# Performance work log

Measured on AMD Instinct MI355X. Metric: run time of the kernel, lower is better.

## Reference

```python
import jax, jax.numpy as jnp
import numpy as np

TAU = 0.07          # softmax temperature
THR = 0.3           # Jaccard similarity threshold for positive pairs
EPS_NORM = 1e-12    # F.normalize eps


def setup_inputs() -> dict:
    key = jax.random.key(0)
    k1, k2, k3 = jax.random.split(key, 3)
    N, D, A = 4096, 128, 512
    z1 = jax.random.normal(k1, (N, D), dtype=jnp.float32)
    z2 = jax.random.normal(k2, (N, D), dtype=jnp.float32)
    labels = jax.random.randint(k3, (N, A), 0, 2).astype(jnp.int32)
    return {"z1": z1, "z2": z2, "labels": labels}


def _l2_normalize(x):
    n = jnp.linalg.norm(x, axis=-1, keepdims=True)
    return x / jnp.maximum(n, EPS_NORM)


def reference(z1, z2, labels):
    # Implements the N > 1000 (chunked) branch of SupConLoss.forward,
    # vectorized over all anchors at once (chunking is just tiling; math identical).
    N = z1.shape[0]
    idx = jnp.arange(N)

    z1n = _l2_normalize(z1)                       # (N, D)
    z2n = _l2_normalize(z2)                       # (N, D)
    z_all = jnp.concatenate([z1n, z2n], axis=0)   # (2N, D)

    # Jaccard label similarity -> positive-pair mask
    lab = labels.astype(jnp.float32)              # (N, A)
    inter = lab @ lab.T                           # (N, N)
    s = lab.sum(axis=1, keepdims=True)            # (N, 1)
    union = s + s.T - inter
    jaccard = inter / (union + 1e-8)
    pos_label = jaccard >= THR                    # (N, N) bool

    # pos mask over 2N columns: label-positives in both halves,
    # augmented view [j, N+j] forced True, self column [j, j] forced False.
    pos_mask = jnp.concatenate([pos_label, pos_label], axis=1)  # (N, 2N)
    pos_mask = pos_mask.at[idx, N + idx].set(True)
    pos_mask = pos_mask.at[idx, idx].set(False)

    # similarity of z1 anchors against all 2N embeddings
    sim = (z1n @ z_all.T) / TAU                   # (N, 2N)
    sim = sim - jax.lax.stop_gradient(sim.max(axis=1, keepdims=True))
    exp_sim = jnp.exp(sim)

    # denominator excludes the self column [j, j]
    denom = exp_sim.sum(axis=1, keepdims=True) - exp_sim[idx, idx][:, None]
    log_prob = sim - jnp.log(denom + 1e-8)

    num_pos = jnp.maximum(pos_mask.sum(axis=1), 1)
    loss_per_sample = -jnp.where(pos_mask, log_prob, 0.0).sum(axis=1) / num_pos
    return loss_per_sample.sum() / N
```

## Files before the change

### kernel.cpp

```cpp
#include <hip/hip_runtime.h>
#include <math.h>

#define N_ROWS 4096
#define DIM    128
#define A_LAB  512
#define INV_TAU 14.285714285714286f
#define C_EXP   20.609929155556620f

typedef __attribute__((ext_vector_type(8))) short short8;
typedef __attribute__((ext_vector_type(4))) float f32x4;
typedef __attribute__((ext_vector_type(4))) int i32x4;
typedef __attribute__((ext_vector_type(16))) int i32x16;


__device__ __forceinline__ unsigned short f2bf(float f) {
  unsigned int u = __builtin_bit_cast(unsigned int, f);
  u += 0x7fffu + ((u >> 16) & 1u);
  return (unsigned short)(u >> 16);
}

__global__ __launch_bounds__(256) void k_norm_pack(
    const float* __restrict__ z1, const float* __restrict__ z2,
    const int* __restrict__ labels,
    unsigned int* __restrict__ zbf, uint2* __restrict__ labs8,
    int* __restrict__ s, float* __restrict__ part, float* __restrict__ out)
{
  {
    const int idx = blockIdx.x * 256 + threadIdx.x;
    if (idx < 3 * 4096) part[idx] = 0.0f;
    if (idx == 0) out[0] = 0.0f;
  }
  const int wave = threadIdx.x >> 6, lane = threadIdx.x & 63;
  const int r = blockIdx.x * 4 + wave;
  const float* src = (r < N_ROWS) ? (z1 + (size_t)r * DIM)
                                  : (z2 + (size_t)(r - N_ROWS) * DIM);
  float2 x = ((const float2*)src)[lane];
  float ss = x.x * x.x + x.y * x.y;
  #pragma unroll
  for (int off = 32; off > 0; off >>= 1) ss += __shfl_xor(ss, off);
  const float inv = 1.0f / fmaxf(sqrtf(ss), 1e-12f);
  const unsigned int lo = f2bf(x.x * inv);
  const unsigned int hi = f2bf(x.y * inv);
  {
    const int u = lane >> 2, p = lane & 3;
    const int kf = u >> 2, quad = u & 3;
    const int g = r >> 4;
    zbf[(size_t)(((g * 4 + kf) * 64) + ((r & 15) + (quad << 4))) * 4 + p] = (hi << 16) | lo;
  }

  if (r < N_ROWS) {
    const int4* lp = (const int4*)(labels + (size_t)r * A_LAB);
    const int4 a = lp[2 * lane], b = lp[2 * lane + 1];
    const unsigned int w0 = (unsigned int)(a.x != 0)       | ((unsigned int)(a.y != 0) << 8)
                          | ((unsigned int)(a.z != 0) << 16) | ((unsigned int)(a.w != 0) << 24);
    const unsigned int w1 = (unsigned int)(b.x != 0)       | ((unsigned int)(b.y != 0) << 8)
                          | ((unsigned int)(b.z != 0) << 16) | ((unsigned int)(b.w != 0) << 24);
    uint2 v; v.x = w0; v.y = w1;
    const int ul = lane >> 1, hp = lane & 1;
    const int ks = ul >> 1, h = ul & 1;
    const int g = r >> 5;
    labs8[(size_t)(((g * 16 + ks) * 64) + ((r & 31) + (h << 5))) * 2 + hp] = v;
    int cnt = __popc(w0) + __popc(w1);
    #pragma unroll
    for (int off = 32; off > 0; off >>= 1) cnt += __shfl_xor(cnt, off);
    if (lane == 0) s[r] = cnt;
  }
}

__global__ __launch_bounds__(512, 4) void k_jac(
    const unsigned char* __restrict__ labs8, const int* __restrict__ s,
    unsigned int* __restrict__ pm)
{
  int r = blockIdx.x, row = 0;
  while (r >= 32 - row) { r -= 32 - row; ++row; }
  const int bi = row, bj = row + r;
  const int ibase = bi * 128, jbase = bj * 128;
  const bool diag = (bi == bj);

  const int tid = threadIdx.x;
  const int wave = tid >> 6, lane = tid & 63;
  const char* gl = (const char*)labs8;

  const int jwr = (wave >> 2) * 64;
  const int jwc = (wave & 3) * 32;
  const int col32 = lane & 31, h = lane >> 5;

  const int s3i = 3 * s[ibase + jwr + lane];
  const int s3j = 3 * s[jbase + jwc + col32];

  i32x16 jacc[2];
  #pragma unroll
  for (int rt = 0; rt < 2; ++rt)
    #pragma unroll
    for (int e = 0; e < 16; ++e) jacc[rt][e] = 0;

  const int gI = (ibase + jwr) >> 5;
  const int gJ = (jbase + jwc) >> 5;
  #pragma unroll
  for (int ks = 0; ks < 16; ++ks) {
    i32x4 a[2], b;
    #pragma unroll
    for (int rt = 0; rt < 2; ++rt)
      a[rt] = *(const i32x4*)(gl + (size_t)(((gI + rt) * 16 + ks) * 64 + lane) * 16);
    b = *(const i32x4*)(gl + (size_t)((gJ * 16 + ks) * 64 + lane) * 16);
    #pragma unroll
    for (int rt = 0; rt < 2; ++rt)
      jacc[rt] = __builtin_amdgcn_mfma_i32_32x32x32_i8(a[rt], b, jacc[rt], 0, 0, 0);
  }

  const int wl = wave & 3;
  const int jw0 = (jbase >> 5);
  unsigned int tw0 = 0, tw1 = 0;
  #pragma unroll
  for (int rt = 0; rt < 2; ++rt)
    #pragma unroll
    for (int reg = 0; reg < 16; ++reg) {
      const int r0 = (reg & 3) + 8 * (reg >> 2);
      const int si = __shfl(s3i, rt * 32 + r0 + 4 * h);
      const bool pred = 13 * jacc[rt][reg] >= si + s3j;
      const unsigned long long bal = __ballot(pred);
      const int lr = jwr + rt * 32 + r0;
      if (lane == 0)      pm[(size_t)(ibase + lr) * 128 + jw0 + wl]       = (unsigned int)bal;
      else if (lane == 1) pm[(size_t)(ibase + lr + 4) * 128 + jw0 + wl]   = (unsigned int)(bal >> 32);
      const unsigned int pb = ((unsigned int)pred) << (r0 + 4 * h);
      if (rt == 0) tw0 |= pb; else tw1 |= pb;
    }
  if (!diag) {
    tw0 |= __shfl_xor(tw0, 32);
    tw1 |= __shfl_xor(tw1, 32);
    const size_t trow = (size_t)(jbase + jwc + col32) * 128 + (ibase >> 5) + (jwr >> 5);
    if (h == 0) pm[trow]     = tw0;
    else        pm[trow + 1] = tw1;
  }
}

__global__ __launch_bounds__(512, 4) void k_fused(
    const unsigned int* __restrict__ pm,
    const unsigned short* __restrict__ zbf, float* __restrict__ part)
{
  __shared__ __align__(16) char bpanel[32768];
  const int tid = threadIdx.x;
  const int ibase = blockIdx.x * 128, jbase = blockIdx.y * 128;
  const int wave = tid >> 6, lane = tid & 63;
  const bool diag = (ibase == jbase);
  const char* gz = (const char*)zbf;

  const int col = lane & 15, quad = lane >> 4;
  const int srow = wave * 16;
  const int gA = (ibase + srow) >> 4;

  uint4 pw[4];
  #pragma unroll
  for (int reg = 0; reg < 4; ++reg)
    pw[reg] = *(const uint4*)&pm[(size_t)(ibase + srow + quad * 4 + reg) * 128 + (jbase >> 5)];

  short8 afr[4];
  #pragma unroll
  for (int kf = 0; kf < 4; ++kf)
    afr[kf] = *(const short8*)(gz + (size_t)((gA * 4 + kf) * 64 + lane) * 16);

  {
    const char* srcp = gz + (size_t)(jbase >> 4) * 4096;
    #pragma unroll
    for (int q = 0; q < 4; ++q)
      *(uint4*)(bpanel + (size_t)(q * 512 + tid) * 16) =
          *(const uint4*)(srcp + (size_t)(q * 512 + tid) * 16);
  }

  __syncthreads();

  float lacc[4], Sacc[4], Pcnt[4];
  #pragma unroll
  for (int reg = 0; reg < 4; ++reg) { lacc[reg] = 0; Sacc[reg] = 0; Pcnt[reg] = 0; }

  #pragma unroll
  for (int half = 0; half < 2; ++half) {
    if (half == 1) {
      __syncthreads();
      const char* srcp = gz + (size_t)((N_ROWS + jbase) >> 4) * 4096;
      #pragma unroll
      for (int q = 0; q < 4; ++q)
        *(uint4*)(bpanel + (size_t)(q * 512 + tid) * 16) =
            *(const uint4*)(srcp + (size_t)(q * 512 + tid) * 16);
      __syncthreads();
    }

    f32x4 acc[8];
    #pragma unroll
    for (int nt = 0; nt < 8; ++nt) acc[nt] = (f32x4){0, 0, 0, 0};

    #pragma unroll
    for (int nt = 0; nt < 8; ++nt) {
      short8 bfr[4];
      #pragma unroll
      for (int kf = 0; kf < 4; ++kf)
        bfr[kf] = *(const short8*)(bpanel + (size_t)((nt * 4 + kf) * 64 + lane) * 16);
      #pragma unroll
      for (int kf = 0; kf < 4; ++kf)
        acc[nt] = __builtin_amdgcn_mfma_f32_16x16x32_bf16(afr[kf], bfr[kf], acc[nt], 0, 0, 0);
    }

    if (!diag) {
      #pragma unroll
      for (int nt = 0; nt < 8; ++nt) {
        const int bitpos = (nt & 1) * 16 + col;
        #pragma unroll
        for (int reg = 0; reg < 4; ++reg) {
          const unsigned int w = ((const unsigned int*)&pw[reg])[nt >> 1];
          const float d = acc[nt][reg];
          lacc[reg] += exp2f(fmaf(d, C_EXP, -C_EXP));
          if ((w >> bitpos) & 1) Sacc[reg] += d;
        }
      }
    } else {
      const bool left = (half == 0);
      #pragma unroll
      for (int nt = 0; nt < 8; ++nt) {
        const int joff = nt * 16 + col;
        const int jc = jbase + joff;
        const int bitpos = joff & 31;
        #pragma unroll
        for (int reg = 0; reg < 4; ++reg) {
          const int i = ibase + srow + quad * 4 + reg;
          const unsigned int w = ((const unsigned int*)&pw[reg])[nt >> 1];
          const float d = acc[nt][reg];
          const bool bit = (w >> bitpos) & 1;
          const bool self = left && (jc == i);
          const bool pos = left ? (bit && !self) : (bit || (jc == i));
          const float e = exp2f(fmaf(d, C_EXP, -C_EXP));
          if (!self) lacc[reg] += e;
          if (pos) { Sacc[reg] += d; Pcnt[reg] += 1.0f; }
        }
      }
    }
  }

  #pragma unroll
  for (int reg = 0; reg < 4; ++reg) {
    float l = lacc[reg], S = Sacc[reg], P = Pcnt[reg];
    #pragma unroll
    for (int m = 1; m < 16; m <<= 1) {
      l += __shfl_xor(l, m);
      S += __shfl_xor(S, m);
      if (diag) P += __shfl_xor(P, m);
    }
    if (col == 0) {
      const int i = ibase + srow + quad * 4 + reg;
      if (!diag) {
        const uint4 w = pw[reg];
        P = 2.0f * (float)(__popc(w.x) + __popc(w.y) + __popc(w.z) + __popc(w.w));
      }
      atomicAdd(&part[i], l);
      atomicAdd(&part[4096 + i], S);
      atomicAdd(&part[8192 + i], P);
    }
  }
}

__global__ __launch_bounds__(128) void k_loss(
    const float* __restrict__ part, float* __restrict__ out)
{
  const int a = blockIdx.x * 128 + threadIdx.x;
  const float l = part[a];
  const float S = part[4096 + a];
  const float P = part[8192 + a];
  const float np = fmaxf(P, 1.0f);
  float v = INV_TAU + logf(l + 1e-8f) - (S * INV_TAU) / np;
  #pragma unroll
  for (int off = 32; off > 0; off >>= 1) v += __shfl_xor(v, off);
  __shared__ float ws2[2];
  const int wave = threadIdx.x >> 6, lane = threadIdx.x & 63;
  if (lane == 0) ws2[wave] = v;
  __syncthreads();
  if (threadIdx.x == 0) atomicAdd(out, (ws2[0] + ws2[1]) * (1.0f / (float)N_ROWS));
}

extern "C" void kernel_launch(void* const* d_in, const int* in_sizes, int n_in,
                              void* d_out, int out_size, void* d_ws, size_t ws_size,
                              hipStream_t stream) {
  const float* z1 = (const float*)d_in[0];
  const float* z2 = (const float*)d_in[1];
  const int* labels = (const int*)d_in[2];
  float* out = (float*)d_out;
  char* ws = (char*)d_ws;

  unsigned int* zbf    = (unsigned int*)(ws);
  uint2* labs8         = (uint2*)(ws + 2097152);
  int* s               = (int*)(ws + 4194304);
  float* part          = (float*)(ws + 4210688);
  unsigned int* pm     = (unsigned int*)(ws + 4259840);

  hipLaunchKernelGGL(k_norm_pack, dim3(2048), dim3(256), 0, stream,
                     z1, z2, labels, zbf, labs8, s, part, out);
  hipLaunchKernelGGL(k_jac, dim3(528), dim3(512), 0, stream,
                     (const unsigned char*)labs8, s, pm);
  hipLaunchKernelGGL(k_fused, dim3(32, 32), dim3(512), 0, stream,
                     pm, (const unsigned short*)zbf, part);
  hipLaunchKernelGGL(k_loss, dim3(32), dim3(128), 0, stream, part, out);
}
```

Baseline: 105.6 us.

## Split fused sim kernel per column half, give each wave two row tiles

The fused similarity/loss kernel now launches one block per 128-column panel across both halves (64x32 grid) instead of one block that loops over the z1 and z2 halves with a mid-kernel reload and extra barriers. Blocks shrink to 256 threads (4 waves), each wave handling two 16-row tiles so every B fragment read from LDS feeds two MFMAs. Diagonal special cases are split into self-diagonal and augmented-diagonal blocks. This doubles block count and the atomic traffic to the partial buffers, and raises register use per wave.

```diff
diff --git a/kernel.cpp b/kernel.cpp
--- a/kernel.cpp
+++ b/kernel.cpp
@@ -134,127 +134,126 @@
   }
 }
 
-__global__ __launch_bounds__(512, 4) void k_fused(
+__global__ __launch_bounds__(256, 3) void k_fused(
     const unsigned int* __restrict__ pm,
     const unsigned short* __restrict__ zbf, float* __restrict__ part)
 {
   __shared__ __align__(16) char bpanel[32768];
   const int tid = threadIdx.x;
-  const int ibase = blockIdx.x * 128, jbase = blockIdx.y * 128;
+  const int cb = blockIdx.x;
+  const int ib = blockIdx.y;
+  const int ibase = ib * 128;
   const int wave = tid >> 6, lane = tid & 63;
-  const bool diag = (ibase == jbase);
+  const int col = lane & 15, quad = lane >> 4;
+  const int wbase = wave * 32;
   const char* gz = (const char*)zbf;
 
-  const int col = lane & 15, quad = lane >> 4;
-  const int srow = wave * 16;
-  const int gA = (ibase + srow) >> 4;
-
-  uint4 pw[4];
-  #pragma unroll
-  for (int reg = 0; reg < 4; ++reg)
-    pw[reg] = *(const uint4*)&pm[(size_t)(ibase + srow + quad * 4 + reg) * 128 + (jbase >> 5)];
-
-  short8 afr[4];
-  #pragma unroll
-  for (int kf = 0; kf < 4; ++kf)
-    afr[kf] = *(const short8*)(gz + (size_t)((gA * 4 + kf) * 64 + lane) * 16);
+  const bool selfd = (cb == ib);
+  const bool augd  = (cb == ib + 32);
+  const bool special = selfd || augd;
 
   {
-    const char* srcp = gz + (size_t)(jbase >> 4) * 4096;
-    #pragma unroll
-    for (int q = 0; q < 4; ++q)
-      *(uint4*)(bpanel + (size_t)(q * 512 + tid) * 16) =
-          *(const uint4*)(srcp + (size_t)(q * 512 + tid) * 16);
-  }
+    const char* srcp = gz + (size_t)cb * 32768;
+    #pragma unroll
+    for (int q = 0; q < 8; ++q)
+      *(uint4*)(bpanel + (size_t)(q * 256 + tid) * 16) =
+          *(const uint4*)(srcp + (size_t)(q * 256 + tid) * 16);
+  }
+
+  short8 afr[2][4];
+  #pragma unroll
+  for (int rt = 0; rt < 2; ++rt) {
+    const int gA = (ibase + wbase + rt * 16) >> 4;
+    #pragma unroll
+    for (int kf = 0; kf < 4; ++kf)
+      afr[rt][kf] = *(const short8*)(gz + (size_t)((gA * 4 + kf) * 64 + lane) * 16);
+  }
+
+  uint4 pw[2][4];
+  #pragma unroll
+  for (int rt = 0; rt < 2; ++rt)
+    #pragma unroll
+    for (int reg = 0; reg < 4; ++reg)
+      pw[rt][reg] = *(const uint4*)&pm[
+          (size_t)(ibase + wbase + rt * 16 + quad * 4 + reg) * 128 + (cb & 31) * 4];
+
+  float lacc[2][4], Sacc[2][4], Pcnt[2][4];
+  #pragma unroll
+  for (int rt = 0; rt < 2; ++rt)
+    #pragma unroll
+    for (int reg = 0; reg < 4; ++reg) { lacc[rt][reg] = 0; Sacc[rt][reg] = 0; Pcnt[rt][reg] = 0; }
 
   __syncthreads();
 
-  float lacc[4], Sacc[4], Pcnt[4];
-  #pragma unroll
-  for (int reg = 0; reg < 4; ++reg) { lacc[reg] = 0; Sacc[reg] = 0; Pcnt[reg] = 0; }
-
-  #pragma unroll
-  for (int half = 0; half < 2; ++half) {
-    if (half == 1) {
-      __syncthreads();
-      const char* srcp = gz + (size_t)((N_ROWS + jbase) >> 4) * 4096;
+  #pragma unroll
+  for (int nt = 0; nt < 8; ++nt) {
+    short8 bfr[4];
+    #pragma unroll
+    for (int kf = 0; kf < 4; ++kf)
+      bfr[kf] = *(const short8*)(bpanel + (size_t)((nt * 4 + kf) * 64 + lane) * 16);
+    f32x4 acc[2];
+    acc[0] = (f32x4){0, 0, 0, 0};
+    acc[1] = (f32x4){0, 0, 0, 0};
+    #pragma unroll
+    for (int kf = 0; kf < 4; ++kf) {
+      acc[0] = __builtin_amdgcn_mfma_f32_16x16x32_bf16(afr[0][kf], bfr[kf], acc[0], 0, 0, 0);
+      acc[1] = __builtin_amdgcn_mfma_f32_16x16x32_bf16(afr[1][kf], bfr[kf], acc[1], 0, 0, 0);
+    }
+
+    if (!special) {
+      const int bitpos = (nt & 1) * 16 + col;
       #pragma unroll
-      for (int q = 0; q < 4; ++q)
-        *(uint4*)(bpanel + (size_t)(q * 512 + tid) * 16) =
-            *(const uint4*)(srcp + (size_t)(q * 512 + tid) * 16);
-      __syncthreads();
-    }
-
-    f32x4 acc[8];
-    #pragma unroll
-    for (int nt = 0; nt < 8; ++nt) acc[nt] = (f32x4){0, 0, 0, 0};
-
-    #pragma unroll
-    for (int nt = 0; nt < 8; ++nt) {
-      short8 bfr[4];
-      #pragma unroll
-      for (int kf = 0; kf < 4; ++kf)
-        bfr[kf] = *(const short8*)(bpanel + (size_t)((nt * 4 + kf) * 64 + lane) * 16);
-      #pragma unroll
-      for (int kf = 0; kf < 4; ++kf)
-        acc[nt] = __builtin_amdgcn_mfma_f32_16x16x32_bf16(afr[kf], bfr[kf], acc[nt], 0, 0, 0);
-    }
-
-    if (!diag) {
-      #pragma unroll
-      for (int nt = 0; nt < 8; ++nt) {
-        const int bitpos = (nt & 1) * 16 + col;
+      for (int rt = 0; rt < 2; ++rt)
         #pragma unroll
         for (int reg = 0; reg < 4; ++reg) {
-          const unsigned int w = ((const unsigned int*)&pw[reg])[nt >> 1];
-          const float d = acc[nt][reg];
-          lacc[reg] += exp2f(fmaf(d, C_EXP, -C_EXP));
-          if ((w >> bitpos) & 1) Sacc[reg] += d;
+          const unsigned int w = ((const unsigned int*)&pw[rt][reg])[nt >> 1];
+          const float d = acc[rt][reg];
+          lacc[rt][reg] += exp2f(fmaf(d, C_EXP, -C_EXP));
+          if ((w >> bitpos) & 1) Sacc[rt][reg] += d;
         }
-      }
     } else {
-      const bool left = (half == 0);
+      const int joff = nt * 16 + col;
+      const int bitpos = joff & 31;
       #pragma unroll
-      for (int nt = 0; nt < 8; ++nt) {
-        const int joff = nt * 16 + col;
-        const int jc = jbase + joff;
-        const int bitpos = joff & 31;
+      for (int rt = 0; rt < 2; ++rt)
         #pragma unroll
         for (int reg = 0; reg < 4; ++reg) {
-          const int i = ibase + srow + quad * 4 + reg;
-          const unsigned int w = ((const unsigned int*)&pw[reg])[nt >> 1];
-          const float d = acc[nt][reg];
+          const int iloc = wbase + rt * 16 + quad * 4 + reg;
+          const unsigned int w = ((const unsigned int*)&pw[rt][reg])[nt >> 1];
+          const float d = acc[rt][reg];
           const bool bit = (w >> bitpos) & 1;
-          const bool self = left && (jc == i);
-          const bool pos = left ? (bit && !self) : (bit || (jc == i));
+          const bool hit = (joff == iloc);
+          const bool self = selfd && hit;
+          const bool pos = selfd ? (bit && !self) : (bit || hit);
           const float e = exp2f(fmaf(d, C_EXP, -C_EXP));
-          if (!self) lacc[reg] += e;
-          if (pos) { Sacc[reg] += d; Pcnt[reg] += 1.0f; }
+          if (!self) lacc[rt][reg] += e;
+          if (pos) { Sacc[rt][reg] += d; Pcnt[rt][reg] += 1.0f; }
         }
+    }
+  }
+
+  #pragma unroll
+  for (int rt = 0; rt < 2; ++rt)
+    #pragma unroll
+    for (int reg = 0; reg < 4; ++reg) {
+      float l = lacc[rt][reg], S = Sacc[rt][reg], P = Pcnt[rt][reg];
+      #pragma unroll
+      for (int m = 1; m < 16; m <<= 1) {
+        l += __shfl_xor(l, m);
+        S += __shfl_xor(S, m);
+        if (special) P += __shfl_xor(P, m);
       }
-    }
-  }
-
-  #pragma unroll
-  for (int reg = 0; reg < 4; ++reg) {
-    float l = lacc[reg], S = Sacc[reg], P = Pcnt[reg];
-    #pragma unroll
-    for (int m = 1; m < 16; m <<= 1) {
-      l += __shfl_xor(l, m);
-      S += __shfl_xor(S, m);
-      if (diag) P += __shfl_xor(P, m);
-    }
-    if (col == 0) {
-      const int i = ibase + srow + quad * 4 + reg;
-      if (!diag) {
-        const uint4 w = pw[reg];
-        P = 2.0f * (float)(__popc(w.x) + __popc(w.y) + __popc(w.z) + __popc(w.w));
+      if (col == 0) {
+        const int i = ibase + wbase + rt * 16 + quad * 4 + reg;
+        if (!special) {
+          const uint4 w = pw[rt][reg];
+          P = (float)(__popc(w.x) + __popc(w.y) + __popc(w.z) + __popc(w.w));
+        }
+        atomicAdd(&part[i], l);
+        atomicAdd(&part[4096 + i], S);
+        atomicAdd(&part[8192 + i], P);
       }
-      atomicAdd(&part[i], l);
-      atomicAdd(&part[4096 + i], S);
-      atomicAdd(&part[8192 + i], P);
-    }
-  }
+    }
 }
 
 __global__ __launch_bounds__(128) void k_loss(
@@ -294,7 +293,7 @@
                      z1, z2, labels, zbf, labs8, s, part, out);
   hipLaunchKernelGGL(k_jac, dim3(528), dim3(512), 0, stream,
                      (const unsigned char*)labs8, s, pm);
-  hipLaunchKernelGGL(k_fused, dim3(32, 32), dim3(512), 0, stream,
+  hipLaunchKernelGGL(k_fused, dim3(64, 32), dim3(256), 0, stream,
                      pm, (const unsigned short*)zbf, part);
   hipLaunchKernelGGL(k_loss, dim3(32), dim3(128), 0, stream, part, out);
 }
```

Result: slower. 138.8 us (+31.4%).
